# Performance work log

Measured on AMD Instinct MI355X. Metric: run time of the kernel, lower is better.

The kernel has to match this reference:

```python
import jax, jax.numpy as jnp
import numpy as np

N_ATOMS = 512
BATCH = 32


def _get_segments(n):
    # shifted pairs (k, k+1), all combinations of 2 rows, drop pairs where end1 == start2
    pairs = np.stack([np.arange(n - 1), np.arange(1, n)], axis=1)  # (n-1, 2)
    i, j = np.triu_indices(n - 1, k=1)
    seg = np.concatenate([pairs[i], pairs[j]], axis=1)  # (M, 4)
    seg = seg[seg[:, 1] != seg[:, 2]]
    return seg.astype(np.int32)  # (129795, 4) for n=512


def setup_inputs() -> dict:
    key = jax.random.key(0)
    x = jax.random.normal(key, (BATCH, N_ATOMS, 3), dtype=jnp.float32) * 5.0
    segments = jnp.asarray(_get_segments(N_ATOMS))
    return {"x": x, "segments": segments}


def _nnorm(v):
    return v / jnp.linalg.norm(v, axis=-1, keepdims=True)


def reference(x, segments):
    n = N_ATOMS
    x = x.reshape(-1, n, 3)
    B = x.shape[0]
    smat = x[:, segments]                       # (B, S, 4, 3) gather
    S = smat.shape[1]
    # displacements between the two segment endpoints pairs: d_{ab} = p_{2+b} - p_a
    disp = _nnorm((-smat[:, :, :2, None, :] + smat[:, :, None, 2:, :]).reshape(B, S, 4, 3))
    crosses = _nnorm(jnp.cross(disp[:, :, [0, 1, 3, 2]], disp[:, :, [1, 3, 2, 0]]))
    omega = jnp.arcsin(
        jnp.clip(jnp.sum(crosses * crosses[:, :, [1, 2, 3, 0]], axis=-1), -1.0, 1.0)
    ).sum(axis=2)                               # (B, S)
    signs = jnp.sign(
        jnp.sum(
            jnp.cross(_nnorm(smat[:, :, 3] - smat[:, :, 2]), _nnorm(smat[:, :, 1] - smat[:, :, 0]))
            * disp[:, :, 0],
            axis=-1,
        )
    )
    wr = (omega * signs) / (2.0 * jnp.pi)       # (B, S)
    # scatter into adjacency matrix (sequential sets: second overrides first, like torch)
    adj = jnp.zeros((B, n, n), dtype=x.dtype)
    adj = adj.at[:, segments[:, 0], segments[:, 2]].set(wr)
    adj = adj.at[:, segments[:, 1], segments[:, 3]].set(wr)
    return adj + jnp.swapaxes(adj, 1, 2)
```

## Files before the change

kernel.cpp:

```cpp
#include <hip/hip_runtime.h>
#include <math.h>

#define N 512
#define TILE 32

struct F3 { float x, y, z; };

__device__ __forceinline__ F3 f3sub(F3 a, F3 b) { return {a.x - b.x, a.y - b.y, a.z - b.z}; }
__device__ __forceinline__ F3 f3cross(F3 a, F3 b) {
    return {a.y * b.z - a.z * b.y, a.z * b.x - a.x * b.z, a.x * b.y - a.y * b.x};
}
__device__ __forceinline__ float f3dot(F3 a, F3 b) { return a.x * b.x + a.y * b.y + a.z * b.z; }

__device__ __forceinline__ float fast_asinf(float x) {
    float ax = fabsf(x);
    float p = fmaf(ax, -0.0187293f, 0.0742610f);
    p = fmaf(ax, p, -0.2121144f);
    p = fmaf(ax, p, 1.5707288f);
    float r = 1.5707963267948966f - __builtin_sqrtf(1.0f - ax) * p;
    return copysignf(r, x);
}

__device__ __forceinline__ float wr_val(const float4* __restrict__ xs4, int a, int b) {
    float4 q0 = xs4[a];
    float4 q1 = xs4[a + 1];
    float4 q2 = xs4[b];
    float4 q3 = xs4[b + 1];
    F3 p0 = {q0.x, q0.y, q0.z};
    F3 p1 = {q1.x, q1.y, q1.z};
    F3 p2 = {q2.x, q2.y, q2.z};
    F3 p3 = {q3.x, q3.y, q3.z};

    F3 d0 = f3sub(p2, p0), d1 = f3sub(p3, p0), d2 = f3sub(p2, p1), d3 = f3sub(p3, p1);

    F3 c0 = f3cross(d0, d1);
    F3 c1 = f3cross(d1, d3);
    F3 c2 = f3cross(d3, d2);
    F3 c3 = f3cross(d2, d0);

    float r0 = rsqrtf(f3dot(c0, c0));
    float r1 = rsqrtf(f3dot(c1, c1));
    float r2 = rsqrtf(f3dot(c2, c2));
    float r3 = rsqrtf(f3dot(c3, c3));

    float t01 = fminf(1.f, fmaxf(-1.f, f3dot(c0, c1) * (r0 * r1)));
    float t12 = fminf(1.f, fmaxf(-1.f, f3dot(c1, c2) * (r1 * r2)));
    float t23 = fminf(1.f, fmaxf(-1.f, f3dot(c2, c3) * (r2 * r3)));
    float t30 = fminf(1.f, fmaxf(-1.f, f3dot(c3, c0) * (r3 * r0)));

    float omega = fast_asinf(t01) + fast_asinf(t12) + fast_asinf(t23) + fast_asinf(t30);

    F3 e = f3cross(f3sub(p3, p2), f3sub(p1, p0));
    float sv = f3dot(e, d0);
    float sgn = (sv > 0.f) ? 1.f : ((sv < 0.f) ? -1.f : 0.f);

    return omega * sgn * 0.15915494309189535f;
}

__global__ __launch_bounds__(256) void writhe_tile(const float* __restrict__ x,
                                                   float* __restrict__ out) {
    __shared__ float4 xs4[N];
    __shared__ float ts[TILE][TILE + 1];

    const int batch = blockIdx.y;
    const float* xb = x + (size_t)batch * (N * 3);
    for (int i = threadIdx.x; i < N; i += blockDim.x) {
        xs4[i] = make_float4(xb[3 * i], xb[3 * i + 1], xb[3 * i + 2], 0.f);
    }

    int p = blockIdx.x;
    int ti = 0;
    while (p >= (N / TILE) - ti) { p -= (N / TILE) - ti; ++ti; }
    const int tj = ti + p;

    __syncthreads();

    const int c = threadIdx.x & 31;
    const int r0 = threadIdx.x >> 5;
    const bool diag = (ti == tj);

    float* ob = out + (size_t)batch * (N * N);

#pragma unroll
    for (int k = 0; k < 4; ++k) {
        const int r = r0 + 8 * k;
        const int gi = ti * TILE + r;
        const int gj = tj * TILE + c;
        const int lo = min(gi, gj), hi = max(gi, gj);
        bool valid;
        int a, b;
        if (lo == 0) { valid = (hi >= 2) && (hi <= 510); a = 0; b = hi; }
        else         { valid = (hi >= lo + 2);           a = lo - 1; b = hi - 1; }
        float v = 0.f;
        if (valid) v = wr_val(xs4, a, b);
        ob[(size_t)gi * N + gj] = v;
        if (!diag) ts[r][c] = v;
    }

    if (!diag) {
        __syncthreads();
#pragma unroll
        for (int k = 0; k < 4; ++k) {
            const int r = r0 + 8 * k;
            ob[(size_t)(tj * TILE + r) * N + (ti * TILE + c)] = ts[c][r];
        }
    }
}

extern "C" void kernel_launch(void* const* d_in, const int* in_sizes, int n_in,
                              void* d_out, int out_size, void* d_ws, size_t ws_size,
                              hipStream_t stream) {
    const float* x = (const float*)d_in[0];
    float* out = (float*)d_out;
    const int B = in_sizes[0] / (N * 3);

    const int ntiles = N / TILE;
    const int npairs = ntiles * (ntiles + 1) / 2;

    dim3 block(256);
    dim3 grid(npairs, B);
    writhe_tile<<<grid, block, 0, stream>>>(x, out);
}
```

Measured before the change: 94.42 us.

## Process several tile pairs per block and vectorize coordinate staging

```diff
diff --git a/kernel.cpp b/kernel.cpp
--- a/kernel.cpp
+++ b/kernel.cpp
@@ -3,6 +3,7 @@
 
 #define N 512
 #define TILE 32
+#define TPB 4
 
 struct F3 { float x, y, z; };
 
@@ -12,25 +13,21 @@
 }
 __device__ __forceinline__ float f3dot(F3 a, F3 b) { return a.x * b.x + a.y * b.y + a.z * b.z; }
 
+__device__ __forceinline__ F3 ldp(const float4* __restrict__ xs4, int i) {
+    float4 q = xs4[i];
+    return {q.x, q.y, q.z};
+}
+
 __device__ __forceinline__ float fast_asinf(float x) {
     float ax = fabsf(x);
     float p = fmaf(ax, -0.0187293f, 0.0742610f);
     p = fmaf(ax, p, -0.2121144f);
     p = fmaf(ax, p, 1.5707288f);
-    float r = 1.5707963267948966f - __builtin_sqrtf(1.0f - ax) * p;
+    float r = 1.5707963267948966f - __builtin_amdgcn_sqrtf(1.0f - ax) * p;
     return copysignf(r, x);
 }
 
-__device__ __forceinline__ float wr_val(const float4* __restrict__ xs4, int a, int b) {
-    float4 q0 = xs4[a];
-    float4 q1 = xs4[a + 1];
-    float4 q2 = xs4[b];
-    float4 q3 = xs4[b + 1];
-    F3 p0 = {q0.x, q0.y, q0.z};
-    F3 p1 = {q1.x, q1.y, q1.z};
-    F3 p2 = {q2.x, q2.y, q2.z};
-    F3 p3 = {q3.x, q3.y, q3.z};
-
+__device__ __forceinline__ float wr_core(F3 p0, F3 p1, F3 p2, F3 p3) {
     F3 d0 = f3sub(p2, p0), d1 = f3sub(p3, p0), d2 = f3sub(p2, p1), d3 = f3sub(p3, p1);
 
     F3 c0 = f3cross(d0, d1);
@@ -59,50 +56,78 @@
 
 __global__ __launch_bounds__(256) void writhe_tile(const float* __restrict__ x,
                                                    float* __restrict__ out) {
-    __shared__ float4 xs4[N];
+    __shared__ __align__(16) float4 xs4[N];
     __shared__ float ts[TILE][TILE + 1];
 
     const int batch = blockIdx.y;
-    const float* xb = x + (size_t)batch * (N * 3);
-    for (int i = threadIdx.x; i < N; i += blockDim.x) {
-        xs4[i] = make_float4(xb[3 * i], xb[3 * i + 1], xb[3 * i + 2], 0.f);
+
+    {
+        const float4* src = (const float4*)(x + (size_t)batch * (N * 3));
+        float* xsf = (float*)xs4;
+        for (int i = threadIdx.x; i < (N * 3) / 4; i += blockDim.x) {
+            float4 g = src[i];
+            const int base = 4 * i;
+            float vv[4] = {g.x, g.y, g.z, g.w};
+#pragma unroll
+            for (int j = 0; j < 4; ++j) {
+                const int e = base + j;
+                xsf[(e / 3) * 4 + (e % 3)] = vv[j];
+            }
+        }
     }
-
-    int p = blockIdx.x;
-    int ti = 0;
-    while (p >= (N / TILE) - ti) { p -= (N / TILE) - ti; ++ti; }
-    const int tj = ti + p;
-
     __syncthreads();
 
     const int c = threadIdx.x & 31;
     const int r0 = threadIdx.x >> 5;
-    const bool diag = (ti == tj);
-
     float* ob = out + (size_t)batch * (N * N);
 
+    for (int t = 0; t < TPB; ++t) {
+        int p = blockIdx.x * TPB + t;
+        int ti = 0;
+        while (p >= (N / TILE) - ti) { p -= (N / TILE) - ti; ++ti; }
+        const int tj = ti + p;
+        const bool diag = (ti == tj);
+        const int gj = tj * TILE + c;
+
+        if (!diag) {
+            const F3 p2 = ldp(xs4, gj - 1);
+            const F3 p3 = ldp(xs4, gj);
 #pragma unroll
-    for (int k = 0; k < 4; ++k) {
-        const int r = r0 + 8 * k;
-        const int gi = ti * TILE + r;
-        const int gj = tj * TILE + c;
-        const int lo = min(gi, gj), hi = max(gi, gj);
-        bool valid;
-        int a, b;
-        if (lo == 0) { valid = (hi >= 2) && (hi <= 510); a = 0; b = hi; }
-        else         { valid = (hi >= lo + 2);           a = lo - 1; b = hi - 1; }
-        float v = 0.f;
-        if (valid) v = wr_val(xs4, a, b);
-        ob[(size_t)gi * N + gj] = v;
-        if (!diag) ts[r][c] = v;
-    }
-
-    if (!diag) {
-        __syncthreads();
+            for (int k = 0; k < 4; ++k) {
+                const int r = r0 + 8 * k;
+                const int gi = ti * TILE + r;
+                float v = 0.f;
+                if (gi == 0) {
+                    if (gj <= 510) {
+                        v = wr_core(ldp(xs4, 0), ldp(xs4, 1), ldp(xs4, gj), ldp(xs4, gj + 1));
+                    }
+                } else if (gj >= gi + 2) {
+                    v = wr_core(ldp(xs4, gi - 1), ldp(xs4, gi), p2, p3);
+                }
+                ob[(size_t)gi * N + gj] = v;
+                ts[r][c] = v;
+            }
+            __syncthreads();
 #pragma unroll
-        for (int k = 0; k < 4; ++k) {
-            const int r = r0 + 8 * k;
-            ob[(size_t)(tj * TILE + r) * N + (ti * TILE + c)] = ts[c][r];
+            for (int k = 0; k < 4; ++k) {
+                const int r = r0 + 8 * k;
+                ob[(size_t)(tj * TILE + r) * N + (ti * TILE + c)] = ts[c][r];
+            }
+            __syncthreads();
+        } else {
+#pragma unroll
+            for (int k = 0; k < 4; ++k) {
+                const int r = r0 + 8 * k;
+                const int gi = ti * TILE + r;
+                const int lo = min(gi, gj), hi = max(gi, gj);
+                bool valid;
+                int a, b;
+                if (lo == 0) { valid = (hi >= 2) && (hi <= 510); a = 0; b = hi; }
+                else         { valid = (hi >= lo + 2);           a = lo - 1; b = hi - 1; }
+                float v = 0.f;
+                if (valid) v = wr_core(ldp(xs4, a), ldp(xs4, a + 1), ldp(xs4, b), ldp(xs4, b + 1));
+                ob[(size_t)gi * N + gj] = v;
+            }
         }
     }
 }
@@ -116,8 +141,9 @@
 
     const int ntiles = N / TILE;
     const int npairs = ntiles * (ntiles + 1) / 2;
+    const int ngroups = (npairs + TPB - 1) / TPB;
 
     dim3 block(256);
-    dim3 grid(npairs, B);
+    dim3 grid(ngroups, B);
     writhe_tile<<<grid, block, 0, stream>>>(x, out);
 }
```

New measurement: 96.32 us. +2.0%, slower.
